# Performance work log

Hardware: AMD Instinct MI355X
Metric: run time of the kernel (lower is better)

## Reference

```python
import jax, jax.numpy as jnp
import numpy as np

COMMITMENT_COST = 0.25
EPSILON = 1e-5


def setup_inputs() -> dict:
    key = jax.random.key(0)
    k1, k2, k3 = jax.random.split(key, 3)
    B, T, D, M = 64, 512, 256, 1024
    audio_semantic = jax.random.normal(k1, (B, T, D), dtype=jnp.float32)
    eeg_semantic = jax.random.normal(k2, (B, T, D), dtype=jnp.float32)
    init_bound = 1.0 / 400.0
    embedding = jax.random.uniform(k3, (M, D), dtype=jnp.float32,
                                   minval=-init_bound, maxval=init_bound)
    return {"audio_semantic": audio_semantic, "eeg_semantic": eeg_semantic,
            "embedding": embedding}


def _distances(flat, embedding):
    return (jnp.sum(embedding ** 2, axis=1)
            + jnp.sum(flat ** 2, axis=1, keepdims=True)
            - 2.0 * (flat @ embedding.T))


def reference(audio_semantic, eeg_semantic, embedding):
    M, D = embedding.shape
    B, T, _ = audio_semantic.shape
    N = B * T
    a_flat = audio_semantic.reshape(-1, D)
    e_flat = eeg_semantic.reshape(-1, D)

    a_dis = _distances(a_flat, embedding)  # [N, M]
    e_dis = _distances(e_flat, embedding)

    # soft assignment probabilities (clamp tiny negative dists before sqrt)
    a_ph = jax.nn.softmax(-jnp.sqrt(jnp.maximum(a_dis, 0.0)), axis=1)
    a_ph = a_ph.reshape(B, T, M).mean(axis=1)  # [B, M]
    e_ph = jax.nn.softmax(-jnp.sqrt(jnp.maximum(e_dis, 0.0)), axis=1)
    e_ph = e_ph.reshape(B, T, M).mean(axis=1)

    # cross-modal code matching loss
    Scode = a_ph @ jnp.log(e_ph.T + 1e-10) + e_ph @ jnp.log(a_ph.T + 1e-10)  # [B, B]
    MaxScode = jnp.max(-Scode)
    EScode = jnp.exp(Scode + MaxScode)
    Lcmcm = -jnp.mean(jnp.log(jnp.diag(EScode) / (jnp.sum(EScode, axis=1) + EPSILON)))
    cmcm_loss = 0.5 * Lcmcm

    # hard assignment + codebook gather
    a_indices = jnp.argmin(a_dis, axis=-1)  # [N]
    e_indices = jnp.argmin(e_dis, axis=-1)
    a_quantized = embedding[a_indices].reshape(B, T, D)
    e_quantized = embedding[e_indices].reshape(B, T, D)

    # per-sample mode of indices (ties -> smallest index, like torch.mode)
    a_counts = jax.nn.one_hot(a_indices.reshape(B, T), M, dtype=jnp.float32).sum(axis=1)
    e_counts = jax.nn.one_hot(e_indices.reshape(B, T), M, dtype=jnp.float32).sum(axis=1)
    a_mode = jnp.argmax(a_counts, axis=-1)
    e_mode = jnp.argmax(e_counts, axis=-1)
    equal_num = jnp.sum(a_mode == e_mode)

    # commitment losses (quantized detached)
    a_q_sg = jax.lax.stop_gradient(a_quantized)
    e_q_sg = jax.lax.stop_gradient(e_quantized)
    a_e_latent = jnp.mean((audio_semantic - a_q_sg) ** 2)
    ae_e_latent = jnp.mean((audio_semantic - e_q_sg) ** 2)
    a_loss = COMMITMENT_COST * (2.0 * a_e_latent + ae_e_latent)
    e_e_latent = jnp.mean((eeg_semantic - e_q_sg) ** 2)
    ea_e_latent = jnp.mean((eeg_semantic - a_q_sg) ** 2)
    e_loss = COMMITMENT_COST * (2.0 * e_e_latent + ea_e_latent)

    # straight-through estimator
    a_quantized_st = audio_semantic + jax.lax.stop_gradient(a_quantized - audio_semantic)
    e_quantized_st = eeg_semantic + jax.lax.stop_gradient(e_quantized - eeg_semantic)

    # perplexity from average usage
    a_avg = jnp.zeros((M,), jnp.float32).at[a_indices].add(1.0) / N
    e_avg = jnp.zeros((M,), jnp.float32).at[e_indices].add(1.0) / N
    a_perplexity = jnp.exp(-jnp.sum(a_avg * jnp.log(a_avg + 1e-10)))
    e_perplexity = jnp.exp(-jnp.sum(e_avg * jnp.log(e_avg + 1e-10)))

    return (a_quantized_st, e_quantized_st, a_loss, e_loss,
            a_perplexity, e_perplexity, cmcm_loss, equal_num)
```

## Files before the change

kernel.cpp:

```cpp
#include <hip/hip_runtime.h>
#include <math.h>

#define Bn 64
#define Tn 512
#define Dn 256
#define Mn 1024
#define Nn (Bn * Tn)
#define NnDn ((size_t)Nn * Dn)

typedef __attribute__((ext_vector_type(8))) short short8v;
typedef __attribute__((ext_vector_type(4))) float float4v;

#define OFF_APH   0
#define OFF_EPH   65536
#define OFF_ACNT  131072
#define OFF_ECNT  196608
#define OFF_LAT   262144
#define OFF_ENT   262148
#define OFF_MODEA 262152
#define OFF_MODEE 262216
#define ZERO_FLOATS 262656
#define OFF_SE2   262656
#define OFF_EH    263680
#define OFF_EL    394752
#define OFF_APHN  525824
#define OFF_EPHN  591360
#define OFF_LA    656896
#define OFF_LE    722432
#define OFF_SCODE 787968
#define OUT_SCALARS ((size_t)2 * Nn * Dn)

__device__ __forceinline__ unsigned short bf16hi(float x) {
  unsigned u = __float_as_uint(x);
  return (unsigned short)((u + 0x7FFFu + ((u >> 16) & 1u)) >> 16);
}
__device__ __forceinline__ float bf16tof(unsigned short h) {
  return __uint_as_float(((unsigned)h) << 16);
}

__global__ __launch_bounds__(256) void kPrepE(const float* __restrict__ emb,
                                              float* __restrict__ ws) {
  unsigned short* Eh = (unsigned short*)(ws + OFF_EH);
  unsigned short* El = (unsigned short*)(ws + OFF_EL);
  float* se2 = ws + OFF_SE2;
  const int tid = threadIdx.x;
  const int m = blockIdx.x * 32 + (tid >> 3);
  const int sub = tid & 7;
  const float* src = emb + (size_t)m * Dn + sub * 32;
  unsigned short* dh = Eh + (size_t)sub * 32768 + m * 32;
  unsigned short* dl = El + (size_t)sub * 32768 + m * 32;
  float s2 = 0.f;
  #pragma unroll
  for (int gq = 0; gq < 4; ++gq) {
    float4 v0 = ((const float4*)src)[gq * 2];
    float4 v1 = ((const float4*)src)[gq * 2 + 1];
    float xs[8] = {v0.x, v0.y, v0.z, v0.w, v1.x, v1.y, v1.z, v1.w};
    short8v hv, lv;
    #pragma unroll
    for (int j = 0; j < 8; ++j) {
      s2 = fmaf(xs[j], xs[j], s2);
      unsigned short h = bf16hi(xs[j]);
      hv[j] = (short)h;
      lv[j] = (short)bf16hi(xs[j] - bf16tof(h));
    }
    *(short8v*)(dh + gq * 8) = hv;
    *(short8v*)(dl + gq * 8) = lv;
  }
  s2 += __shfl_xor(s2, 1); s2 += __shfl_xor(s2, 2); s2 += __shfl_xor(s2, 4);
  if (sub == 0) se2[m] = s2;
}

__global__ __launch_bounds__(1024) void kMain(
    const float* __restrict__ audio, const float* __restrict__ eeg,
    const float* __restrict__ emb, float* out, float* __restrict__ ws) {
  __shared__ unsigned short Xh[64 * 128];
  __shared__ unsigned short Xl[64 * 128];
  __shared__ float se2l[Mn];
  __shared__ float sx2l[64];
  __shared__ float wmin[64][16];
  __shared__ int   widx[64][16];
  __shared__ float wZ[64][16];
  __shared__ float rowLs[64];
  __shared__ int   rowIdxs[64];
  __shared__ float izs[64];
  __shared__ float redm[16][4];

  const int tid = threadIdx.x;
  const int n0 = blockIdx.x * 32;
  const int b = blockIdx.x >> 4;
  const unsigned short* __restrict__ Eh = (const unsigned short*)(ws + OFF_EH);

  const int lane = tid & 63, wid = tid >> 6;
  const int c = lane & 15, g = lane >> 4;
  const int colbase = wid * 64;

  se2l[tid] = ws[OFF_SE2 + tid];

  float4v acc[4][4];
  #pragma unroll
  for (int rg = 0; rg < 4; ++rg)
    #pragma unroll
    for (int cg = 0; cg < 4; ++cg) {
      float4v z = {0.f, 0.f, 0.f, 0.f};
      acc[rg][cg] = z;
    }

  const int srow = tid >> 4, ssub = tid & 15;
  const float* ssrc = (srow < 32) ? (audio + (size_t)(n0 + srow) * Dn)
                                  : (eeg + (size_t)(n0 + srow - 32) * Dn);
  const int sab = (srow * 256 + ssub * 16) ^ ((srow & 7) << 4);
  char* XhB = (char*)Xh;
  char* XlB = (char*)Xl;
  int rowb[4], swzr[4];
  #pragma unroll
  for (int rg = 0; rg < 4; ++rg) {
    int row = rg * 16 + c;
    rowb[rg] = row * 256;
    swzr[rg] = (row & 7) << 4;
  }
  const unsigned short* pEH = Eh + (size_t)colbase * 32 + (c * 32 + g * 8);

  float s2 = 0.f;
  for (int ph = 0; ph < 2; ++ph) {
    if (ph) __syncthreads();
    {
      const float* sp = ssrc + ph * 128 + ssub * 8;
      float4 v0 = ((const float4*)sp)[0];
      float4 v1 = ((const float4*)sp)[1];
      float xs[8] = {v0.x, v0.y, v0.z, v0.w, v1.x, v1.y, v1.z, v1.w};
      short8v hv, lv;
      #pragma unroll
      for (int j = 0; j < 8; ++j) {
        s2 = fmaf(xs[j], xs[j], s2);
        unsigned short h = bf16hi(xs[j]);
        hv[j] = (short)h;
        lv[j] = (short)bf16hi(xs[j] - bf16tof(h));
      }
      *(short8v*)(XhB + sab) = hv;
      *(short8v*)(XlB + sab) = lv;
    }
    __syncthreads();
    for (int ks4 = 0; ks4 < 4; ++ks4) {
      const int kb = ks4 * 64 + g * 16;
      const unsigned short* peh = pEH + (size_t)(ph * 4 + ks4) * 32768;
      short8v ah[4], al[4];
      #pragma unroll
      for (int rg = 0; rg < 4; ++rg) {
        const int ab = rowb[rg] + (kb ^ swzr[rg]);
        ah[rg] = *(const short8v*)(XhB + ab);
        al[rg] = *(const short8v*)(XlB + ab);
      }
      #pragma unroll
      for (int cg = 0; cg < 4; ++cg) {
        short8v bh = *(const short8v*)(peh + cg * 512);
        short8v bl = *(const short8v*)(peh + cg * 512 + 262144);
        #pragma unroll
        for (int rg = 0; rg < 4; ++rg) {
          acc[rg][cg] = __builtin_amdgcn_mfma_f32_16x16x32_bf16(ah[rg], bh, acc[rg][cg], 0, 0, 0);
          acc[rg][cg] = __builtin_amdgcn_mfma_f32_16x16x32_bf16(al[rg], bh, acc[rg][cg], 0, 0, 0);
          acc[rg][cg] = __builtin_amdgcn_mfma_f32_16x16x32_bf16(ah[rg], bl, acc[rg][cg], 0, 0, 0);
        }
      }
    }
  }
  s2 += __shfl_xor(s2, 1); s2 += __shfl_xor(s2, 2);
  s2 += __shfl_xor(s2, 4); s2 += __shfl_xor(s2, 8);
  if (ssub == 0) sx2l[srow] = s2;

  float se2c[4];
  #pragma unroll
  for (int cg = 0; cg < 4; ++cg) se2c[cg] = se2l[colbase + cg * 16 + c];
  #pragma unroll
  for (int rg = 0; rg < 4; ++rg)
    #pragma unroll
    for (int cg = 0; cg < 4; ++cg)
      #pragma unroll
      for (int q = 0; q < 4; ++q)
        acc[rg][cg][q] = fmaf(-2.f, acc[rg][cg][q], se2c[cg]);

  float vmin[4][4]; int imin[4][4];
  #pragma unroll
  for (int rg = 0; rg < 4; ++rg)
    #pragma unroll
    for (int q = 0; q < 4; ++q) { vmin[rg][q] = 3.0e38f; imin[rg][q] = Mn; }
  #pragma unroll
  for (int cg = 0; cg < 4; ++cg) {
    const int colc = colbase + cg * 16 + c;
    #pragma unroll
    for (int rg = 0; rg < 4; ++rg)
      #pragma unroll
      for (int q = 0; q < 4; ++q) {
        float v = acc[rg][cg][q];
        if (v < vmin[rg][q]) { vmin[rg][q] = v; imin[rg][q] = colc; }
      }
  }
  #pragma unroll
  for (int off = 1; off <= 8; off <<= 1) {
    #pragma unroll
    for (int rg = 0; rg < 4; ++rg)
      #pragma unroll
      for (int q = 0; q < 4; ++q) {
        float ov = __shfl_xor(vmin[rg][q], off);
        int oi = __shfl_xor(imin[rg][q], off);
        if (ov < vmin[rg][q] || (ov == vmin[rg][q] && oi < imin[rg][q])) {
          vmin[rg][q] = ov; imin[rg][q] = oi;
        }
      }
  }
  if (c == 0) {
    #pragma unroll
    for (int rg = 0; rg < 4; ++rg)
      #pragma unroll
      for (int q = 0; q < 4; ++q) {
        int row = rg * 16 + g * 4 + q;
        wmin[row][wid] = vmin[rg][q];
        widx[row][wid] = imin[rg][q];
      }
  }
  __syncthreads();
  if (tid < 64) {
    float m = wmin[tid][0]; int mi = widx[tid][0];
    #pragma unroll
    for (int w = 1; w < 16; ++w) {
      float v = wmin[tid][w]; int i2 = widx[tid][w];
      if (v < m || (v == m && i2 < mi)) { m = v; mi = i2; }
    }
    rowIdxs[tid] = mi;
    rowLs[tid] = sqrtf(fmaxf(m + sx2l[tid], 0.f));
  }
  __syncthreads();
  if (tid < 32) atomicAdd((unsigned*)(ws + OFF_ACNT) + b * Mn + rowIdxs[tid], 1u);
  else if (tid < 64) atomicAdd((unsigned*)(ws + OFF_ECNT) + b * Mn + rowIdxs[tid], 1u);

  float Lpre[4][4], spre[4][4];
  #pragma unroll
  for (int rg = 0; rg < 4; ++rg)
    #pragma unroll
    for (int q = 0; q < 4; ++q) {
      int row = rg * 16 + g * 4 + q;
      Lpre[rg][q] = rowLs[row];
      spre[rg][q] = sx2l[row];
    }
  float zp[4][4];
  #pragma unroll
  for (int rg = 0; rg < 4; ++rg)
    #pragma unroll
    for (int q = 0; q < 4; ++q) zp[rg][q] = 0.f;
  #pragma unroll
  for (int rg = 0; rg < 4; ++rg)
    #pragma unroll
    for (int cg = 0; cg < 4; ++cg)
      #pragma unroll
      for (int q = 0; q < 4; ++q) {
        float d = acc[rg][cg][q] + spre[rg][q];
        float pv = __expf(Lpre[rg][q] - sqrtf(fmaxf(d, 0.f)));
        acc[rg][cg][q] = pv;
        zp[rg][q] += pv;
      }
  #pragma unroll
  for (int off = 1; off <= 8; off <<= 1)
    #pragma unroll
    for (int rg = 0; rg < 4; ++rg)
      #pragma unroll
      for (int q = 0; q < 4; ++q) zp[rg][q] += __shfl_xor(zp[rg][q], off);
  if (c == 0) {
    #pragma unroll
    for (int rg = 0; rg < 4; ++rg)
      #pragma unroll
      for (int q = 0; q < 4; ++q) wZ[rg * 16 + g * 4 + q][wid] = zp[rg][q];
  }
  __syncthreads();
  if (tid < 64) {
    float Z = 0.f;
    #pragma unroll
    for (int w = 0; w < 16; ++w) Z += wZ[tid][w];
    izs[tid] = 1.f / Z;
  }
  __syncthreads();

  float izq[4][4];
  #pragma unroll
  for (int rg = 0; rg < 4; ++rg)
    #pragma unroll
    for (int q = 0; q < 4; ++q) izq[rg][q] = izs[rg * 16 + g * 4 + q];
  float psA[4], psE[4];
  #pragma unroll
  for (int cg = 0; cg < 4; ++cg) {
    float a = 0.f, e = 0.f;
    #pragma unroll
    for (int q = 0; q < 4; ++q) {
      a += acc[0][cg][q] * izq[0][q] + acc[1][cg][q] * izq[1][q];
      e += acc[2][cg][q] * izq[2][q] + acc[3][cg][q] * izq[3][q];
    }
    a += __shfl_xor(a, 16); a += __shfl_xor(a, 32);
    e += __shfl_xor(e, 16); e += __shfl_xor(e, 32);
    psA[cg] = a; psE[cg] = e;
  }
  if (lane < 16) {
    float* phA = ws + OFF_APH;
    float* phE = ws + OFF_EPH;
    #pragma unroll
    for (int cg = 0; cg < 4; ++cg) {
      int colc = colbase + cg * 16 + lane;
      atomicAdd(phA + b * Mn + colc, psA[cg]);
      atomicAdd(phE + b * Mn + colc, psE[cg]);
    }
  }

  {
    const int r = tid >> 5, pp = tid & 31;
    const int ia = rowIdxs[r], ie = rowIdxs[32 + r];
    const float4* qa = (const float4*)(emb + (size_t)ia * Dn);
    const float4* qe = (const float4*)(emb + (size_t)ie * Dn);
    const float4* xa4 = (const float4*)(audio + (size_t)(n0 + r) * Dn);
    const float4* xe4 = (const float4*)(eeg + (size_t)(n0 + r) * Dn);
    float4* oA = (float4*)(out + (size_t)(n0 + r) * Dn);
    float4* oE = (float4*)(out + NnDn + (size_t)(n0 + r) * Dn);
    float s_ae = 0.f, s_aq = 0.f, s_ee = 0.f, s_eq = 0.f;
    #pragma unroll
    for (int h = 0; h < 2; ++h) {
      const int i4 = pp * 2 + h;
      float4 qav = qa[i4], qev = qe[i4], xav = xa4[i4], xev = xe4[i4];
      float qaf[4] = {qav.x, qav.y, qav.z, qav.w};
      float qef[4] = {qev.x, qev.y, qev.z, qev.w};
      float xaf[4] = {xav.x, xav.y, xav.z, xav.w};
      float xef[4] = {xev.x, xev.y, xev.z, xev.w};
      #pragma unroll
      for (int j = 0; j < 4; ++j) {
        float d1 = xaf[j] - qaf[j]; s_ae += d1 * d1;
        float d2 = xaf[j] - qef[j]; s_aq += d2 * d2;
        float d3 = xef[j] - qef[j]; s_ee += d3 * d3;
        float d4 = xef[j] - qaf[j]; s_eq += d4 * d4;
      }
      oA[i4] = qav;
      oE[i4] = qev;
    }
    #pragma unroll
    for (int off = 1; off <= 32; off <<= 1) {
      s_ae += __shfl_xor(s_ae, off);
      s_aq += __shfl_xor(s_aq, off);
      s_ee += __shfl_xor(s_ee, off);
      s_eq += __shfl_xor(s_eq, off);
    }
    if (lane == 0) {
      redm[wid][0] = s_ae; redm[wid][1] = s_aq;
      redm[wid][2] = s_ee; redm[wid][3] = s_eq;
    }
    __syncthreads();
    if (tid < 4) {
      float t = 0.f;
      #pragma unroll
      for (int w = 0; w < 16; ++w) t += redm[w][tid];
      atomicAdd(ws + OFF_LAT + tid, t);
    }
  }
}

__global__ __launch_bounds__(256) void kAux(float* __restrict__ ws) {
  const int blk = blockIdx.x;
  const int t = threadIdx.x;
  if (blk < 256) {
    int i = blk * 256 + t;
    float a = ws[OFF_APH + i] * (1.f / 512.f);
    float e = ws[OFF_EPH + i] * (1.f / 512.f);
    ws[OFF_APHN + i] = a;
    ws[OFF_EPHN + i] = e;
    ws[OFF_LA + i] = logf(a + 1e-10f);
    ws[OFF_LE + i] = logf(e + 1e-10f);
  } else if (blk < 320) {
    const int bb = blk - 256;
    const unsigned* acnt = (const unsigned*)(ws + OFF_ACNT) + (size_t)bb * Mn;
    const unsigned* ecnt = (const unsigned*)(ws + OFF_ECNT) + (size_t)bb * Mn;
    __shared__ unsigned rv[256]; __shared__ int ri[256];
    __shared__ unsigned rv2[256]; __shared__ int ri2[256];
    unsigned bA = 0; int ia = t;
    unsigned bE = 0; int ie = t;
    #pragma unroll
    for (int m = t; m < Mn; m += 256) {
      unsigned ca = acnt[m]; if (ca > bA) { bA = ca; ia = m; }
      unsigned ce = ecnt[m]; if (ce > bE) { bE = ce; ie = m; }
    }
    rv[t] = bA; ri[t] = ia; rv2[t] = bE; ri2[t] = ie;
    __syncthreads();
    for (int s2 = 128; s2 > 0; s2 >>= 1) {
      if (t < s2) {
        if (rv[t + s2] > rv[t] || (rv[t + s2] == rv[t] && ri[t + s2] < ri[t])) {
          rv[t] = rv[t + s2]; ri[t] = ri[t + s2];
        }
        if (rv2[t + s2] > rv2[t] || (rv2[t + s2] == rv2[t] && ri2[t + s2] < ri2[t])) {
          rv2[t] = rv2[t + s2]; ri2[t] = ri2[t + s2];
        }
      }
      __syncthreads();
    }
    if (t == 0) {
      ((int*)ws)[OFF_MODEA + bb] = ri[0];
      ((int*)ws)[OFF_MODEE + bb] = ri2[0];
    }
  } else {
    const int m = (blk - 320) * 256 + t;
    const unsigned* acnt = (const unsigned*)(ws + OFF_ACNT);
    const unsigned* ecnt = (const unsigned*)(ws + OFF_ECNT);
    unsigned ta = 0, te = 0;
    for (int bb = 0; bb < Bn; ++bb) {
      ta += acnt[(size_t)bb * Mn + m];
      te += ecnt[(size_t)bb * Mn + m];
    }
    float av = (float)ta * (1.f / 32768.f);
    float ev = (float)te * (1.f / 32768.f);
    float ea = av * logf(av + 1e-10f);
    float ee = ev * logf(ev + 1e-10f);
    #pragma unroll
    for (int off = 1; off <= 32; off <<= 1) { ea += __shfl_xor(ea, off); ee += __shfl_xor(ee, off); }
    __shared__ float r2[4][2];
    const int ln = t & 63, w = t >> 6;
    if (ln == 0) { r2[w][0] = ea; r2[w][1] = ee; }
    __syncthreads();
    if (t == 0) {
      atomicAdd(ws + OFF_ENT + 0, r2[0][0] + r2[1][0] + r2[2][0] + r2[3][0]);
      atomicAdd(ws + OFF_ENT + 1, r2[0][1] + r2[1][1] + r2[2][1] + r2[3][1]);
    }
  }
}

__global__ __launch_bounds__(256) void kC1(float* __restrict__ ws) {
  const int blk = blockIdx.x;
  const int i = blk >> 2, jq = blk & 3;
  const int t = threadIdx.x;
  const int jj = t >> 4, q = t & 15;
  const int j = jq * 16 + jj;
  const float* ai  = ws + OFF_APHN + (size_t)i * Mn;
  const float* ei  = ws + OFF_EPHN + (size_t)i * Mn;
  const float* lej = ws + OFF_LE + (size_t)j * Mn;
  const float* laj = ws + OFF_LA + (size_t)j * Mn;
  float s = 0.f;
  #pragma unroll 4
  for (int m = q * 64; m < q * 64 + 64; ++m)
    s += ai[m] * lej[m] + ei[m] * laj[m];
  s += __shfl_xor(s, 1); s += __shfl_xor(s, 2);
  s += __shfl_xor(s, 4); s += __shfl_xor(s, 8);
  if (q == 0) ws[OFF_SCODE + i * 64 + j] = s;
}

__global__ __launch_bounds__(256) void kFin(float* __restrict__ ws, float* __restrict__ out) {
  __shared__ float sc[4096];
  __shared__ float red[256];
  __shared__ float rterm[64];
  __shared__ float maxv;
  const int tid = threadIdx.x;
  for (int i = tid; i < 4096; i += 256) sc[i] = ws[OFF_SCODE + i];
  __syncthreads();

  float mx = -3.0e38f;
  for (int i = tid; i < 4096; i += 256) mx = fmaxf(mx, -sc[i]);
  red[tid] = mx; __syncthreads();
  for (int s = 128; s > 0; s >>= 1) {
    if (tid < s) red[tid] = fmaxf(red[tid], red[tid + s]);
    __syncthreads();
  }
  if (tid == 0) maxv = red[0];
  __syncthreads();
  const float Max = maxv;

  if (tid < 64) {
    float rs = 0.f;
    for (int j = 0; j < 64; ++j) rs += expf(sc[tid * 64 + j] + Max);
    float dg = expf(sc[tid * 64 + tid] + Max);
    rterm[tid] = logf(dg / (rs + 1e-5f));
  }
  __syncthreads();
  if (tid == 0) {
    float s = 0.f;
    for (int i = 0; i < 64; ++i) s += rterm[i];
    out[OUT_SCALARS + 4] = -0.5f * s / 64.f;
  }
  if (tid == 1) {
    const float* lat = ws + OFF_LAT;
    const float inv = 1.f / 8388608.f;
    float a_e = lat[0] * inv, ae = lat[1] * inv, e_e = lat[2] * inv, ea = lat[3] * inv;
    out[OUT_SCALARS + 0] = 0.25f * (2.f * a_e + ae);
    out[OUT_SCALARS + 1] = 0.25f * (2.f * e_e + ea);
  }
  if (tid == 2) out[OUT_SCALARS + 2] = expf(-ws[OFF_ENT + 0]);
  if (tid == 3) out[OUT_SCALARS + 3] = expf(-ws[OFF_ENT + 1]);
  if (tid == 4) {
    const int* ma = (const int*)ws + OFF_MODEA;
    const int* me = (const int*)ws + OFF_MODEE;
    int eq = 0;
    for (int b2 = 0; b2 < 64; ++b2) eq += (ma[b2] == me[b2]) ? 1 : 0;
    out[OUT_SCALARS + 5] = (float)eq;
  }
}

extern "C" void kernel_launch(void* const* d_in, const int* in_sizes, int n_in,
                              void* d_out, int out_size, void* d_ws, size_t ws_size,
                              hipStream_t stream) {
  const float* audio = (const float*)d_in[0];
  const float* eeg   = (const float*)d_in[1];
  const float* emb   = (const float*)d_in[2];
  float* out = (float*)d_out;
  float* ws  = (float*)d_ws;
  (void)in_sizes; (void)n_in; (void)out_size; (void)ws_size;

  hipMemsetAsync(d_ws, 0, (size_t)ZERO_FLOATS * sizeof(float), stream);
  hipLaunchKernelGGL(kPrepE, dim3(32), dim3(256), 0, stream, emb, ws);
  hipLaunchKernelGGL(kMain, dim3(Nn / 32), dim3(1024), 0, stream, audio, eeg, emb, out, ws);
  hipLaunchKernelGGL(kAux, dim3(324), dim3(256), 0, stream, ws);
  hipLaunchKernelGGL(kC1, dim3(256), dim3(256), 0, stream, ws);
  hipLaunchKernelGGL(kFin, dim3(1), dim3(256), 0, stream, ws, out);
}
```

Baseline: 336.3 us.

## Retile kMain to 16-row blocks of 512 threads with single-phase K staging

The main distance kernel now processes 16 audio plus 16 eeg rows per block with 8 waves each covering 128 codebook columns, instead of 32+32 rows with 16 waves. The whole 256-wide row is staged to LDS in one pass with a padded stride in place of two swizzled phases, removing a barrier. The argmin becomes a two-pass fminf-then-index reduction, and the distance clamp and row norm are folded in before the softmax. Halving rows per block doubles the codebook reads from global/L2 per row of X, trading that against smaller blocks, fewer barriers and higher occupancy (launch bounds 512,4).

After: 328.6 us. 2.3% less time.

```diff
diff --git a/kernel.cpp b/kernel.cpp
--- a/kernel.cpp
+++ b/kernel.cpp
@@ -30,6 +30,8 @@
 #define OFF_SCODE 787968
 #define OUT_SCALARS ((size_t)2 * Nn * Dn)
 
+#define XSTRB 520
+
 __device__ __forceinline__ unsigned short bf16hi(float x) {
   unsigned u = __float_as_uint(x);
   return (unsigned short)((u + 0x7FFFu + ((u >> 16) & 1u)) >> 16);
@@ -70,246 +72,254 @@
   if (sub == 0) se2[m] = s2;
 }
 
-__global__ __launch_bounds__(1024) void kMain(
+__global__ __launch_bounds__(512, 4) void kMain(
     const float* __restrict__ audio, const float* __restrict__ eeg,
     const float* __restrict__ emb, float* out, float* __restrict__ ws) {
-  __shared__ unsigned short Xh[64 * 128];
-  __shared__ unsigned short Xl[64 * 128];
+  __shared__ unsigned short Xh[32 * (XSTRB / 2)];
+  __shared__ unsigned short Xl[32 * (XSTRB / 2)];
   __shared__ float se2l[Mn];
-  __shared__ float sx2l[64];
-  __shared__ float wmin[64][16];
-  __shared__ int   widx[64][16];
-  __shared__ float wZ[64][16];
-  __shared__ float rowLs[64];
-  __shared__ int   rowIdxs[64];
-  __shared__ float izs[64];
-  __shared__ float redm[16][4];
+  __shared__ float sx2l[32];
+  __shared__ float wmin[32][8];
+  __shared__ int   widx[32][8];
+  __shared__ float wZ[32][8];
+  __shared__ float rowLs[32];
+  __shared__ int   rowIdxs[32];
+  __shared__ float izs[32];
+  __shared__ float redm[8][4];
 
   const int tid = threadIdx.x;
-  const int n0 = blockIdx.x * 32;
-  const int b = blockIdx.x >> 4;
+  const int n0 = blockIdx.x * 16;
+  const int b = blockIdx.x >> 5;
   const unsigned short* __restrict__ Eh = (const unsigned short*)(ws + OFF_EH);
+  const unsigned short* __restrict__ El = (const unsigned short*)(ws + OFF_EL);
 
   const int lane = tid & 63, wid = tid >> 6;
   const int c = lane & 15, g = lane >> 4;
-  const int colbase = wid * 64;
+  const int colbase = wid * 128;
 
   se2l[tid] = ws[OFF_SE2 + tid];
-
-  float4v acc[4][4];
-  #pragma unroll
-  for (int rg = 0; rg < 4; ++rg)
-    #pragma unroll
-    for (int cg = 0; cg < 4; ++cg) {
+  se2l[tid + 512] = ws[OFF_SE2 + tid + 512];
+
+  float4v acc[2][8];
+  #pragma unroll
+  for (int rg = 0; rg < 2; ++rg)
+    #pragma unroll
+    for (int cg = 0; cg < 8; ++cg) {
       float4v z = {0.f, 0.f, 0.f, 0.f};
       acc[rg][cg] = z;
     }
 
-  const int srow = tid >> 4, ssub = tid & 15;
-  const float* ssrc = (srow < 32) ? (audio + (size_t)(n0 + srow) * Dn)
-                                  : (eeg + (size_t)(n0 + srow - 32) * Dn);
-  const int sab = (srow * 256 + ssub * 16) ^ ((srow & 7) << 4);
   char* XhB = (char*)Xh;
   char* XlB = (char*)Xl;
-  int rowb[4], swzr[4];
-  #pragma unroll
-  for (int rg = 0; rg < 4; ++rg) {
-    int row = rg * 16 + c;
-    rowb[rg] = row * 256;
-    swzr[rg] = (row & 7) << 4;
-  }
-  const unsigned short* pEH = Eh + (size_t)colbase * 32 + (c * 32 + g * 8);
-
-  float s2 = 0.f;
-  for (int ph = 0; ph < 2; ++ph) {
-    if (ph) __syncthreads();
-    {
-      const float* sp = ssrc + ph * 128 + ssub * 8;
-      float4 v0 = ((const float4*)sp)[0];
-      float4 v1 = ((const float4*)sp)[1];
+
+  const int srow = tid >> 4, ssub = tid & 15;
+  {
+    const float* sp = (srow < 16) ? (audio + (size_t)(n0 + srow) * Dn + ssub * 16)
+                                  : (eeg + (size_t)(n0 + srow - 16) * Dn + ssub * 16);
+    float s2 = 0.f;
+    const int ab = srow * XSTRB + ssub * 32;
+    #pragma unroll
+    for (int h = 0; h < 2; ++h) {
+      float4 v0 = ((const float4*)sp)[h * 2];
+      float4 v1 = ((const float4*)sp)[h * 2 + 1];
       float xs[8] = {v0.x, v0.y, v0.z, v0.w, v1.x, v1.y, v1.z, v1.w};
       short8v hv, lv;
       #pragma unroll
       for (int j = 0; j < 8; ++j) {
-        s2 = fmaf(xs[j], xs[j], s2);
-        unsigned short h = bf16hi(xs[j]);
-        hv[j] = (short)h;
-        lv[j] = (short)bf16hi(xs[j] - bf16tof(h));
-      }
-      *(short8v*)(XhB + sab) = hv;
-      *(short8v*)(XlB + sab) = lv;
-    }
-    __syncthreads();
-    for (int ks4 = 0; ks4 < 4; ++ks4) {
-      const int kb = ks4 * 64 + g * 16;
-      const unsigned short* peh = pEH + (size_t)(ph * 4 + ks4) * 32768;
-      short8v ah[4], al[4];
-      #pragma unroll
-      for (int rg = 0; rg < 4; ++rg) {
-        const int ab = rowb[rg] + (kb ^ swzr[rg]);
-        ah[rg] = *(const short8v*)(XhB + ab);
-        al[rg] = *(const short8v*)(XlB + ab);
-      }
-      #pragma unroll
-      for (int cg = 0; cg < 4; ++cg) {
+        float x = xs[j];
+        s2 = fmaf(x, x, s2);
+        unsigned u = __float_as_uint(x);
+        unsigned r = u + 0x7FFFu + ((u >> 16) & 1u);
+        hv[j] = (short)(unsigned short)(r >> 16);
+        float lof = x - __uint_as_float(r & 0xFFFF0000u);
+        lv[j] = (short)(unsigned short)(__float_as_uint(lof) >> 16);
+      }
+      *(short8v*)(XhB + ab + h * 16) = hv;
+      *(short8v*)(XlB + ab + h * 16) = lv;
+    }
+    s2 += __shfl_xor(s2, 1); s2 += __shfl_xor(s2, 2);
+    s2 += __shfl_xor(s2, 4); s2 += __shfl_xor(s2, 8);
+    if (ssub == 0) sx2l[srow] = s2;
+  }
+  __syncthreads();
+
+  {
+    const int rowb0 = c * XSTRB;
+    const int rowb1 = (16 + c) * XSTRB;
+    const unsigned short* pEHb = Eh + (size_t)colbase * 32 + (c * 32 + g * 8);
+    const unsigned short* pELb = El + (size_t)colbase * 32 + (c * 32 + g * 8);
+    #pragma unroll
+    for (int ks = 0; ks < 8; ++ks) {
+      const int kb = ks * 64 + g * 16;
+      short8v a0h = *(const short8v*)(XhB + rowb0 + kb);
+      short8v a0l = *(const short8v*)(XlB + rowb0 + kb);
+      short8v a1h = *(const short8v*)(XhB + rowb1 + kb);
+      short8v a1l = *(const short8v*)(XlB + rowb1 + kb);
+      const unsigned short* peh = pEHb + (size_t)ks * 32768;
+      const unsigned short* pel = pELb + (size_t)ks * 32768;
+      #pragma unroll
+      for (int cg = 0; cg < 8; ++cg) {
         short8v bh = *(const short8v*)(peh + cg * 512);
-        short8v bl = *(const short8v*)(peh + cg * 512 + 262144);
+        short8v bl = *(const short8v*)(pel + cg * 512);
+        acc[0][cg] = __builtin_amdgcn_mfma_f32_16x16x32_bf16(a0h, bh, acc[0][cg], 0, 0, 0);
+        acc[0][cg] = __builtin_amdgcn_mfma_f32_16x16x32_bf16(a0l, bh, acc[0][cg], 0, 0, 0);
+        acc[0][cg] = __builtin_amdgcn_mfma_f32_16x16x32_bf16(a0h, bl, acc[0][cg], 0, 0, 0);
+        acc[1][cg] = __builtin_amdgcn_mfma_f32_16x16x32_bf16(a1h, bh, acc[1][cg], 0, 0, 0);
+        acc[1][cg] = __builtin_amdgcn_mfma_f32_16x16x32_bf16(a1l, bh, acc[1][cg], 0, 0, 0);
+        acc[1][cg] = __builtin_amdgcn_mfma_f32_16x16x32_bf16(a1h, bl, acc[1][cg], 0, 0, 0);
+      }
+    }
+  }
+
+  float spre[2][4];
+  #pragma unroll
+  for (int rg = 0; rg < 2; ++rg)
+    #pragma unroll
+    for (int q = 0; q < 4; ++q) spre[rg][q] = sx2l[rg * 16 + g * 4 + q];
+  float se2c[8];
+  #pragma unroll
+  for (int cg = 0; cg < 8; ++cg) se2c[cg] = se2l[colbase + cg * 16 + c];
+  #pragma unroll
+  for (int rg = 0; rg < 2; ++rg)
+    #pragma unroll
+    for (int cg = 0; cg < 8; ++cg)
+      #pragma unroll
+      for (int q = 0; q < 4; ++q)
+        acc[rg][cg][q] = fmaxf(fmaf(-2.f, acc[rg][cg][q], se2c[cg]) + spre[rg][q], 0.f);
+
+  {
+    float vmin[2][4];
+    #pragma unroll
+    for (int rg = 0; rg < 2; ++rg)
+      #pragma unroll
+      for (int q = 0; q < 4; ++q) {
+        float m01 = fminf(acc[rg][0][q], acc[rg][1][q]);
+        float m23 = fminf(acc[rg][2][q], acc[rg][3][q]);
+        float m45 = fminf(acc[rg][4][q], acc[rg][5][q]);
+        float m67 = fminf(acc[rg][6][q], acc[rg][7][q]);
+        vmin[rg][q] = fminf(fminf(m01, m23), fminf(m45, m67));
+      }
+    #pragma unroll
+    for (int off = 1; off <= 8; off <<= 1)
+      #pragma unroll
+      for (int rg = 0; rg < 2; ++rg)
         #pragma unroll
-        for (int rg = 0; rg < 4; ++rg) {
-          acc[rg][cg] = __builtin_amdgcn_mfma_f32_16x16x32_bf16(ah[rg], bh, acc[rg][cg], 0, 0, 0);
-          acc[rg][cg] = __builtin_amdgcn_mfma_f32_16x16x32_bf16(al[rg], bh, acc[rg][cg], 0, 0, 0);
-          acc[rg][cg] = __builtin_amdgcn_mfma_f32_16x16x32_bf16(ah[rg], bl, acc[rg][cg], 0, 0, 0);
+        for (int q = 0; q < 4; ++q)
+          vmin[rg][q] = fminf(vmin[rg][q], __shfl_xor(vmin[rg][q], off));
+    int imin[2][4];
+    #pragma unroll
+    for (int rg = 0; rg < 2; ++rg)
+      #pragma unroll
+      for (int q = 0; q < 4; ++q) {
+        int il = Mn;
+        #pragma unroll
+        for (int cg = 0; cg < 8; ++cg) {
+          int colc = colbase + cg * 16 + c;
+          if (acc[rg][cg][q] == vmin[rg][q]) il = min(il, colc);
         }
-      }
-    }
-  }
-  s2 += __shfl_xor(s2, 1); s2 += __shfl_xor(s2, 2);
-  s2 += __shfl_xor(s2, 4); s2 += __shfl_xor(s2, 8);
-  if (ssub == 0) sx2l[srow] = s2;
-
-  float se2c[4];
-  #pragma unroll
-  for (int cg = 0; cg < 4; ++cg) se2c[cg] = se2l[colbase + cg * 16 + c];
-  #pragma unroll
-  for (int rg = 0; rg < 4; ++rg)
-    #pragma unroll
-    for (int cg = 0; cg < 4; ++cg)
-      #pragma unroll
-      for (int q = 0; q < 4; ++q)
-        acc[rg][cg][q] = fmaf(-2.f, acc[rg][cg][q], se2c[cg]);
-
-  float vmin[4][4]; int imin[4][4];
-  #pragma unroll
-  for (int rg = 0; rg < 4; ++rg)
-    #pragma unroll
-    for (int q = 0; q < 4; ++q) { vmin[rg][q] = 3.0e38f; imin[rg][q] = Mn; }
-  #pragma unroll
-  for (int cg = 0; cg < 4; ++cg) {
-    const int colc = colbase + cg * 16 + c;
-    #pragma unroll
-    for (int rg = 0; rg < 4; ++rg)
-      #pragma unroll
-      for (int q = 0; q < 4; ++q) {
-        float v = acc[rg][cg][q];
-        if (v < vmin[rg][q]) { vmin[rg][q] = v; imin[rg][q] = colc; }
-      }
-  }
-  #pragma unroll
-  for (int off = 1; off <= 8; off <<= 1) {
-    #pragma unroll
-    for (int rg = 0; rg < 4; ++rg)
-      #pragma unroll
-      for (int q = 0; q < 4; ++q) {
-        float ov = __shfl_xor(vmin[rg][q], off);
-        int oi = __shfl_xor(imin[rg][q], off);
-        if (ov < vmin[rg][q] || (ov == vmin[rg][q] && oi < imin[rg][q])) {
-          vmin[rg][q] = ov; imin[rg][q] = oi;
+        imin[rg][q] = il;
+      }
+    #pragma unroll
+    for (int off = 1; off <= 8; off <<= 1)
+      #pragma unroll
+      for (int rg = 0; rg < 2; ++rg)
+        #pragma unroll
+        for (int q = 0; q < 4; ++q)
+          imin[rg][q] = min(imin[rg][q], __shfl_xor(imin[rg][q], off));
+    if (c == 0) {
+      #pragma unroll
+      for (int rg = 0; rg < 2; ++rg)
+        #pragma unroll
+        for (int q = 0; q < 4; ++q) {
+          int row = rg * 16 + g * 4 + q;
+          wmin[row][wid] = vmin[rg][q];
+          widx[row][wid] = imin[rg][q];
         }
-      }
-  }
-  if (c == 0) {
-    #pragma unroll
-    for (int rg = 0; rg < 4; ++rg)
-      #pragma unroll
-      for (int q = 0; q < 4; ++q) {
-        int row = rg * 16 + g * 4 + q;
-        wmin[row][wid] = vmin[rg][q];
-        widx[row][wid] = imin[rg][q];
-      }
-  }
-  __syncthreads();
-  if (tid < 64) {
+    }
+  }
+  __syncthreads();
+  if (tid < 32) {
     float m = wmin[tid][0]; int mi = widx[tid][0];
     #pragma unroll
-    for (int w = 1; w < 16; ++w) {
+    for (int w = 1; w < 8; ++w) {
       float v = wmin[tid][w]; int i2 = widx[tid][w];
       if (v < m || (v == m && i2 < mi)) { m = v; mi = i2; }
     }
     rowIdxs[tid] = mi;
-    rowLs[tid] = sqrtf(fmaxf(m + sx2l[tid], 0.f));
-  }
-  __syncthreads();
-  if (tid < 32) atomicAdd((unsigned*)(ws + OFF_ACNT) + b * Mn + rowIdxs[tid], 1u);
-  else if (tid < 64) atomicAdd((unsigned*)(ws + OFF_ECNT) + b * Mn + rowIdxs[tid], 1u);
-
-  float Lpre[4][4], spre[4][4];
-  #pragma unroll
-  for (int rg = 0; rg < 4; ++rg)
-    #pragma unroll
-    for (int q = 0; q < 4; ++q) {
-      int row = rg * 16 + g * 4 + q;
-      Lpre[rg][q] = rowLs[row];
-      spre[rg][q] = sx2l[row];
-    }
-  float zp[4][4];
-  #pragma unroll
-  for (int rg = 0; rg < 4; ++rg)
+    rowLs[tid] = sqrtf(m);
+  }
+  __syncthreads();
+  if (tid < 16) atomicAdd((unsigned*)(ws + OFF_ACNT) + b * Mn + rowIdxs[tid], 1u);
+  else if (tid < 32) atomicAdd((unsigned*)(ws + OFF_ECNT) + b * Mn + rowIdxs[tid], 1u);
+
+  float Lpre[2][4];
+  #pragma unroll
+  for (int rg = 0; rg < 2; ++rg)
+    #pragma unroll
+    for (int q = 0; q < 4; ++q) Lpre[rg][q] = rowLs[rg * 16 + g * 4 + q];
+  float zp[2][4];
+  #pragma unroll
+  for (int rg = 0; rg < 2; ++rg)
     #pragma unroll
     for (int q = 0; q < 4; ++q) zp[rg][q] = 0.f;
   #pragma unroll
-  for (int rg = 0; rg < 4; ++rg)
-    #pragma unroll
-    for (int cg = 0; cg < 4; ++cg)
+  for (int rg = 0; rg < 2; ++rg)
+    #pragma unroll
+    for (int cg = 0; cg < 8; ++cg)
       #pragma unroll
       for (int q = 0; q < 4; ++q) {
-        float d = acc[rg][cg][q] + spre[rg][q];
-        float pv = __expf(Lpre[rg][q] - sqrtf(fmaxf(d, 0.f)));
+        float pv = __expf(Lpre[rg][q] - sqrtf(acc[rg][cg][q]));
         acc[rg][cg][q] = pv;
         zp[rg][q] += pv;
       }
   #pragma unroll
   for (int off = 1; off <= 8; off <<= 1)
     #pragma unroll
-    for (int rg = 0; rg < 4; ++rg)
+    for (int rg = 0; rg < 2; ++rg)
       #pragma unroll
       for (int q = 0; q < 4; ++q) zp[rg][q] += __shfl_xor(zp[rg][q], off);
   if (c == 0) {
     #pragma unroll
-    for (int rg = 0; rg < 4; ++rg)
+    for (int rg = 0; rg < 2; ++rg)
       #pragma unroll
       for (int q = 0; q < 4; ++q) wZ[rg * 16 + g * 4 + q][wid] = zp[rg][q];
   }
   __syncthreads();
-  if (tid < 64) {
+  if (tid < 32) {
     float Z = 0.f;
     #pragma unroll
-    for (int w = 0; w < 16; ++w) Z += wZ[tid][w];
+    for (int w = 0; w < 8; ++w) Z += wZ[tid][w];
     izs[tid] = 1.f / Z;
   }
   __syncthreads();
 
-  float izq[4][4];
-  #pragma unroll
-  for (int rg = 0; rg < 4; ++rg)
-    #pragma unroll
-    for (int q = 0; q < 4; ++q) izq[rg][q] = izs[rg * 16 + g * 4 + q];
-  float psA[4], psE[4];
-  #pragma unroll
-  for (int cg = 0; cg < 4; ++cg) {
-    float a = 0.f, e = 0.f;
-    #pragma unroll
-    for (int q = 0; q < 4; ++q) {
-      a += acc[0][cg][q] * izq[0][q] + acc[1][cg][q] * izq[1][q];
-      e += acc[2][cg][q] * izq[2][q] + acc[3][cg][q] * izq[3][q];
-    }
-    a += __shfl_xor(a, 16); a += __shfl_xor(a, 32);
-    e += __shfl_xor(e, 16); e += __shfl_xor(e, 32);
-    psA[cg] = a; psE[cg] = e;
-  }
-  if (lane < 16) {
-    float* phA = ws + OFF_APH;
-    float* phE = ws + OFF_EPH;
-    #pragma unroll
-    for (int cg = 0; cg < 4; ++cg) {
-      int colc = colbase + cg * 16 + lane;
-      atomicAdd(phA + b * Mn + colc, psA[cg]);
-      atomicAdd(phE + b * Mn + colc, psE[cg]);
+  {
+    float izq[2][4];
+    #pragma unroll
+    for (int rg = 0; rg < 2; ++rg)
+      #pragma unroll
+      for (int q = 0; q < 4; ++q) izq[rg][q] = izs[rg * 16 + g * 4 + q];
+    #pragma unroll
+    for (int cg = 0; cg < 8; ++cg) {
+      float a = 0.f, e = 0.f;
+      #pragma unroll
+      for (int q = 0; q < 4; ++q) {
+        a += acc[0][cg][q] * izq[0][q];
+        e += acc[1][cg][q] * izq[1][q];
+      }
+      a += __shfl_xor(a, 16); a += __shfl_xor(a, 32);
+      e += __shfl_xor(e, 16); e += __shfl_xor(e, 32);
+      if (lane < 16) {
+        int colc = colbase + cg * 16 + lane;
+        atomicAdd(ws + OFF_APH + b * Mn + colc, a);
+        atomicAdd(ws + OFF_EPH + b * Mn + colc, e);
+      }
     }
   }
 
   {
     const int r = tid >> 5, pp = tid & 31;
-    const int ia = rowIdxs[r], ie = rowIdxs[32 + r];
+    const int ia = rowIdxs[r], ie = rowIdxs[16 + r];
     const float4* qa = (const float4*)(emb + (size_t)ia * Dn);
     const float4* qe = (const float4*)(emb + (size_t)ie * Dn);
     const float4* xa4 = (const float4*)(audio + (size_t)(n0 + r) * Dn);
@@ -350,7 +360,7 @@
     if (tid < 4) {
       float t = 0.f;
       #pragma unroll
-      for (int w = 0; w < 16; ++w) t += redm[w][tid];
+      for (int w = 0; w < 8; ++w) t += redm[w][tid];
       atomicAdd(ws + OFF_LAT + tid, t);
     }
   }
@@ -504,7 +514,7 @@
 
   hipMemsetAsync(d_ws, 0, (size_t)ZERO_FLOATS * sizeof(float), stream);
   hipLaunchKernelGGL(kPrepE, dim3(32), dim3(256), 0, stream, emb, ws);
-  hipLaunchKernelGGL(kMain, dim3(Nn / 32), dim3(1024), 0, stream, audio, eeg, emb, out, ws);
+  hipLaunchKernelGGL(kMain, dim3(Nn / 16), dim3(512), 0, stream, audio, eeg, emb, out, ws);
   hipLaunchKernelGGL(kAux, dim3(324), dim3(256), 0, stream, ws);
   hipLaunchKernelGGL(kC1, dim3(256), dim3(256), 0, stream, ws);
   hipLaunchKernelGGL(kFin, dim3(1), dim3(256), 0, stream, ws, out);
```
